# Kernel optimization log

Hardware: AMD Instinct MI355X
Metric: run time of the kernel (lower is better)

The kernel has to match this reference:

```python
import math
import jax, jax.numpy as jnp
import numpy as np

D, H, NB, L, K = 45, 256, 6, 2, 8          # features, hidden, maf blocks, made hidden layers, spline bins
M = 3 * K - 1                               # params per feature (tails='linear')
TAIL = -math.log(1e-6)                      # tail_bound = -log(alpha)
MIN_BW = MIN_BH = MIN_D = 1e-3


def _masks():
    # nflows MADE sequential degrees (random_mask=False)
    d_in = np.arange(1, D + 1)
    d_h = (np.arange(H) % (D - 1)) + 1
    m0 = (d_h[:, None] >= d_in[None, :]).astype(np.float32)   # [H, D]
    mh = (d_h[:, None] >= d_h[None, :]).astype(np.float32)    # [H, H]
    d_out = np.repeat(d_in, M)                                 # nflows tile(): each degree repeated M times
    mf = (d_out[:, None] > d_h[None, :]).astype(np.float32)   # [D*M, H], strict for output layer
    return jnp.asarray(m0), jnp.asarray(mh), jnp.asarray(mf)


def _rq_spline(x, params):
    # x: [B, D]; params: [B, D, M]. unconstrained_rational_quadratic_spline, tails='linear'.
    uw = params[..., :K] / math.sqrt(H)        # nflows divides by sqrt(hidden_features)
    uh = params[..., K:2 * K] / math.sqrt(H)
    const = math.log(math.exp(1.0 - MIN_D) - 1.0)
    ud = jnp.pad(params[..., 2 * K:], ((0, 0), (0, 0), (1, 1)), constant_values=const)  # [B,D,K+1]
    inside = (x >= -TAIL) & (x <= TAIL)
    xc = jnp.clip(x, -TAIL, TAIL)

    def bin_edges(u, mn):
        p = jax.nn.softmax(u, -1)
        p = mn + (1.0 - mn * K) * p
        c = jnp.pad(jnp.cumsum(p, -1), ((0, 0), (0, 0), (1, 0)))
        c = 2.0 * TAIL * c - TAIL
        c = c.at[..., 0].set(-TAIL).at[..., -1].set(TAIL)
        return c, c[..., 1:] - c[..., :-1]

    cw, w = bin_edges(uw, MIN_BW)              # cumwidths [B,D,K+1], widths [B,D,K]
    ch, h = bin_edges(uh, MIN_BH)
    d = MIN_D + jax.nn.softplus(ud)            # derivatives [B,D,K+1]

    idx = jnp.clip(jnp.sum((xc[..., None] >= cw), -1) - 1, 0, K - 1)[..., None]
    g = lambda a: jnp.take_along_axis(a, idx, -1)[..., 0]
    icw, ibw, ich, ih = g(cw[..., :-1]), g(w), g(ch[..., :-1]), g(h)
    idelta = g(h / w)
    id0, id1 = g(d[..., :-1]), g(d[..., 1:])

    th = (xc - icw) / ibw
    th1 = th * (1.0 - th)
    den = idelta + (id0 + id1 - 2.0 * idelta) * th1
    y = ich + ih * (idelta * th * th + id0 * th1) / den
    lad = jnp.log(idelta * idelta * (id1 * th * th + 2.0 * idelta * th1 + id0 * (1.0 - th) ** 2)) - 2.0 * jnp.log(den)
    return jnp.where(inside, y, x), jnp.where(inside, lad, 0.0)


def setup_inputs() -> dict:
    key = jax.random.key(0)
    ks = jax.random.split(key, 10)
    B, s = 32768, 0.02
    return {
        "x": jax.random.normal(ks[0], (B, D), jnp.float32),
        "cond": jax.random.normal(ks[1], (B, 1), jnp.float32),
        "W0": jax.random.normal(ks[2], (NB, H, D), jnp.float32) * s,
        "b0": jax.random.normal(ks[3], (NB, H), jnp.float32) * s,
        "Wc": jax.random.normal(ks[4], (NB, H, 1), jnp.float32) * s,
        "bc": jax.random.normal(ks[5], (NB, H), jnp.float32) * s,
        "Wh": jax.random.normal(ks[6], (NB, L, H, H), jnp.float32) * s,
        "bh": jax.random.normal(ks[7], (NB, L, H), jnp.float32) * s,
        "Wf": jax.random.normal(ks[8], (NB, D * M, H), jnp.float32) * s,
        "bf": jax.random.normal(ks[9], (NB, D * M), jnp.float32) * s,
    }


def reference(x, cond, W0, b0, Wc, bc, Wh, bh, Wf, bf):
    m0, mh, mf = _masks()
    z = x
    ld = jnp.zeros(x.shape[0], x.dtype)
    for b in range(NB):  # CompositeTransform of NB MAF blocks
        hid = z @ (W0[b] * m0).T + b0[b] + cond @ Wc[b].T + bc[b]
        for l in range(L):  # MaskedFeedforwardBlock: linear -> ReLU (dropout=0, no BN)
            hid = jax.nn.relu(hid @ (Wh[b, l] * mh).T + bh[b, l])
        params = (hid @ (Wf[b] * mf).T + bf[b]).reshape(z.shape[0], D, M)
        z, lad = _rq_spline(z, params)
        ld = ld + lad.sum(-1)
    log_z = 0.5 * D * math.log(2.0 * math.pi)
    return -0.5 * jnp.sum(z * z, axis=1) - log_z + ld
```

## Files before the change

kernel.cpp:

```cpp
#include <hip/hip_runtime.h>


typedef __bf16 bf16;
typedef __bf16 bf16x8 __attribute__((ext_vector_type(8)));
typedef float  f32x16 __attribute__((ext_vector_type(16)));

#define TAILF  13.815510557964274f
#define LOGZ   41.352233994210265f

#define WS_W0M   0
#define WS_WHM   196608
#define WS_WFM   1769472
#define WS_BEFF  5210112
#define WS_BFP   5216256
#define WS_WCC   5243136
#define WS_BHP   5249280
#define WS_NEED  5261568

#define N_W0  (6*256*64)
#define N_WH  (6*2*256*256)
#define N_WF  (6*5*224*256)
#define N_PREP (N_W0 + N_WH + N_WF)

__device__ __forceinline__ int s_deg(int s) {
    return (s < 216) ? (s / 6) : (36 + (s - 216) / 5);
}
__device__ __forceinline__ int s_orig(int s) {
    int d, rk;
    if (s < 216) { d = s / 6; rk = s - d * 6; }
    else { int u = s - 216; d = 36 + u / 5; rk = u - (u / 5) * 5; }
    return d + 44 * rk;
}

__global__ void prep_all(const float* __restrict__ W0, const float* __restrict__ b0,
                         const float* __restrict__ Wc, const float* __restrict__ bc,
                         const float* __restrict__ Wh, const float* __restrict__ Wf,
                         const float* __restrict__ bfv, const float* __restrict__ bh,
                         bf16* __restrict__ W0m, bf16* __restrict__ Whm,
                         bf16* __restrict__ Wfm,
                         float* __restrict__ beff, float* __restrict__ bfp,
                         float* __restrict__ Wcc, float* __restrict__ bhp)
{
    int idx = blockIdx.x * 256 + threadIdx.x;
    if (idx < N_W0) {
        int j = idx & 7, lane = (idx >> 3) & 63, chunk = idx >> 9;
        int kt = chunk & 3, cg = (chunk >> 2) & 7, b = chunk >> 5;
        int col = cg * 32 + (lane & 31);
        int k   = kt * 16 + (lane >> 5) * 8 + j;
        int o   = s_orig(col);
        float v = 0.f;
        if (k < 45 && s_deg(col) >= k)
            v = W0[(b * 256 + o) * 45 + k];
        W0m[idx] = (bf16)v;
        if (k == 0) {
            beff[b * 256 + col] = b0[b * 256 + o] + bc[b * 256 + o];
            Wcc[b * 256 + col]  = Wc[b * 256 + o];
        }
    } else if (idx < N_W0 + N_WH) {
        int id = idx - N_W0;
        int j = id & 7, lane = (id >> 3) & 63, chunk = id >> 9;
        int kt = chunk & 15, cg = (chunk >> 4) & 7, bl = chunk >> 7;
        int col = cg * 32 + (lane & 31);
        int k   = kt * 16 + (lane >> 5) * 8 + j;
        int oc  = s_orig(col), ok = s_orig(k);
        float v = (s_deg(col) >= s_deg(k)) ? Wh[bl * 65536 + oc * 256 + ok] : 0.f;
        Whm[id] = (bf16)v;
        if (k == 0)
            bhp[bl * 256 + col] = bh[bl * 256 + oc];
    } else if (idx < N_PREP) {
        int id = idx - (N_W0 + N_WH);
        int j = id & 7, lane = (id >> 3) & 63, chunk = id >> 9;
        int kt = chunk & 15, t2 = chunk >> 4;
        int cg = t2 % 7, bg = t2 / 7;
        int b  = bg / 5, g = bg - 5 * b;
        int col = cg * 32 + (lane & 31);
        int k   = kt * 16 + (lane >> 5) * 8 + j;
        int ok  = s_orig(k);
        int f   = 9 * g + col / 23;
        int m   = col - (col / 23) * 23;
        bool valid = (col < 207);
        float v = 0.f;
        if (valid && (f > s_deg(k)))
            v = Wf[(b * 1035 + f * 23 + m) * 256 + ok];
        Wfm[id] = (bf16)v;
        if (k == 0)
            bfp[bg * 224 + col] = valid ? bfv[b * 1035 + f * 23 + m] : 0.f;
    }
}

#define SO_ZF    0
#define SO_ZB    11776
#define SO_HIDA  18944
#define SO_PBUF  52736
#define SO_COND  80528
#define SO_LD    80784
#define SMEM_BYTES 81040

#define PBF 1544

__constant__ unsigned char HID_KT[8]    = {4,8,8,12,12,12,16,16};
__constant__ unsigned char OUT_KT[5][7] = {
    { 4, 4, 4, 4, 4, 4, 4},
    { 4, 8, 8, 8, 8, 8, 8},
    { 8, 8,12,12,12,12,12},
    {12,12,12,12,16,16,16},
    {16,16,16,16,16,16,16}};

template<int MODE>
__device__ __forceinline__ void epi32(const f32x16& acc, int cg, int hf,
    const float* __restrict__ bias, const float* __restrict__ wcol,
    const float* condl, bf16* dst, int l31, int kh8)
{
    const int col = cg * 32 + l31;
    if (MODE == 2 && col >= 207) return;
    const float bv = bias[col];
    const int rb = (kh8 >> 1) + hf * 32;
    if (MODE == 2) {
        const int fl = col / 23, m = col - fl * 23;
        bf16* dp = dst + fl * PBF + m;
        #pragma unroll
        for (int r = 0; r < 16; ++r) {
            int row = (r & 3) + 8 * (r >> 2) + rb;
            dp[row * 24] = (bf16)(acc[r] + bv);
        }
    } else {
        const float wcv = (MODE == 0) ? wcol[col] : 0.f;
        #pragma unroll
        for (int r = 0; r < 16; ++r) {
            int row = (r & 3) + 8 * (r >> 2) + rb;
            float v = acc[r] + bv;
            if (MODE == 0) v += condl[row] * wcv;
            if (MODE == 1) v = fmaxf(v, 0.f);
            dst[row * 264 + col] = (bf16)v;
        }
    }
}

template<int KTFULL, int MODE>
__device__ __forceinline__ void gemm64(
    const bf16* Asrc, const int lda,
    const bf16* __restrict__ Wp,
    const float* __restrict__ bias, const float* __restrict__ wcol,
    const float* condl, bf16* dst,
    int cg, int kt, int halfmask,
    int lane, bool preEpiSync)
{
    const int l31 = lane & 31;
    const int kh8 = (lane >> 5) * 8;
    const bf16* Bp  = Wp + (size_t)cg * (KTFULL * 512) + lane * 8;
    const bf16* Alo = Asrc + l31 * lda + kh8;
    const bf16* Ahi = Alo + 32 * lda;

    f32x16 acc0 = {}, acc1 = {};
    bf16x8 pA0, pA1, pA2, pA3, pB0, pB1, pB2, pB3;

#define LB(c)  (*reinterpret_cast<const bf16x8*>(Bp + (c) * 512))
#define LAL(c) (*reinterpret_cast<const bf16x8*>(Alo + (c) * 16))
#define LAH(c) (*reinterpret_cast<const bf16x8*>(Ahi + (c) * 16))
#define CHUNK(breg, c) { \
    bf16x8 a0_ = LAL(c), a1_ = LAH(c); \
    acc0 = __builtin_amdgcn_mfma_f32_32x32x16_bf16(a0_, breg, acc0, 0, 0, 0); \
    acc1 = __builtin_amdgcn_mfma_f32_32x32x16_bf16(a1_, breg, acc1, 0, 0, 0); }
#define LOADQ(r0, r1, r2, r3, q) { \
    r0 = LB((q)*4 + 0); r1 = LB((q)*4 + 1); \
    r2 = LB((q)*4 + 2); r3 = LB((q)*4 + 3); }
#define COMPQ(r0, r1, r2, r3, q) { \
    CHUNK(r0, (q)*4 + 0) CHUNK(r1, (q)*4 + 1) \
    CHUNK(r2, (q)*4 + 2) CHUNK(r3, (q)*4 + 3) }

    const int nq = __builtin_amdgcn_readfirstlane(kt >> 2);
    switch (nq) {
    case 1:
        LOADQ(pA0,pA1,pA2,pA3, 0);
        COMPQ(pA0,pA1,pA2,pA3, 0);
        break;
    case 2:
        LOADQ(pA0,pA1,pA2,pA3, 0); LOADQ(pB0,pB1,pB2,pB3, 1);
        COMPQ(pA0,pA1,pA2,pA3, 0); COMPQ(pB0,pB1,pB2,pB3, 1);
        break;
    case 3:
        LOADQ(pA0,pA1,pA2,pA3, 0); LOADQ(pB0,pB1,pB2,pB3, 1);
        COMPQ(pA0,pA1,pA2,pA3, 0); LOADQ(pA0,pA1,pA2,pA3, 2);
        COMPQ(pB0,pB1,pB2,pB3, 1); COMPQ(pA0,pA1,pA2,pA3, 2);
        break;
    default:
        LOADQ(pA0,pA1,pA2,pA3, 0); LOADQ(pB0,pB1,pB2,pB3, 1);
        COMPQ(pA0,pA1,pA2,pA3, 0); LOADQ(pA0,pA1,pA2,pA3, 2);
        COMPQ(pB0,pB1,pB2,pB3, 1); LOADQ(pB0,pB1,pB2,pB3, 3);
        COMPQ(pA0,pA1,pA2,pA3, 2); COMPQ(pB0,pB1,pB2,pB3, 3);
        break;
    }
#undef LB
#undef LAL
#undef LAH
#undef CHUNK
#undef LOADQ
#undef COMPQ

    if (preEpiSync) __syncthreads();

    if (halfmask & 1) epi32<MODE>(acc0, cg, 0, bias, wcol, condl, dst, l31, kh8);
    if (halfmask & 2) epi32<MODE>(acc1, cg, 1, bias, wcol, condl, dst, l31, kh8);
    __syncthreads();
}

__device__ __forceinline__ void do_spline9(int fb, float* zf, bf16* zb,
                                           const bf16* pbuf, int t, float& lad_acc)
{
    #pragma unroll 1
    for (int task = t; task < 576; task += 512) {
        int fl = task >> 6, r = task & 63;
        const bf16* pp = pbuf + fl * PBF + r * 24;
        bf16x8 q0 = *reinterpret_cast<const bf16x8*>(pp);
        bf16x8 q1 = *reinterpret_cast<const bf16x8*>(pp + 8);
        bf16x8 q2 = *reinterpret_cast<const bf16x8*>(pp + 16);
        float P[23];
        #pragma unroll
        for (int m = 0; m < 8; ++m) P[m]      = (float)q0[m];
        #pragma unroll
        for (int m = 0; m < 8; ++m) P[8 + m]  = (float)q1[m];
        #pragma unroll
        for (int m = 0; m < 7; ++m) P[16 + m] = (float)q2[m];

        float xin = zf[r * 46 + fb + fl];
        float xc  = fminf(fmaxf(xin, -TAILF), TAILF);
        bool inside = (xin >= -TAILF) && (xin <= TAILF);

        float mw = P[0];
        #pragma unroll
        for (int i = 1; i < 8; ++i) mw = fmaxf(mw, P[i]);
        float ew[8], sw = 0.f;
        #pragma unroll
        for (int i = 0; i < 8; ++i) { ew[i] = __expf((P[i] - mw) * 0.0625f); sw += ew[i]; }
        float rws = 0.992f / sw;
        float cw[9]; cw[0] = -TAILF;
        #pragma unroll
        for (int i = 0; i < 8; ++i)
            cw[i + 1] = cw[i] + 2.f * TAILF * (1e-3f + ew[i] * rws);
        cw[8] = TAILF;
        float wb[8];
        #pragma unroll
        for (int i = 0; i < 8; ++i) wb[i] = cw[i + 1] - cw[i];

        float mh = P[8];
        #pragma unroll
        for (int i = 1; i < 8; ++i) mh = fmaxf(mh, P[8 + i]);
        float eh[8], sh = 0.f;
        #pragma unroll
        for (int i = 0; i < 8; ++i) { eh[i] = __expf((P[8 + i] - mh) * 0.0625f); sh += eh[i]; }
        float rhs = 0.992f / sh;
        float ch[9]; ch[0] = -TAILF;
        #pragma unroll
        for (int i = 0; i < 8; ++i)
            ch[i + 1] = ch[i] + 2.f * TAILF * (1e-3f + eh[i] * rhs);
        ch[8] = TAILF;
        float hb[8];
        #pragma unroll
        for (int i = 0; i < 8; ++i) hb[i] = ch[i + 1] - ch[i];

        float dd[9];
        dd[0] = 1.0f; dd[8] = 1.0f;
        #pragma unroll
        for (int i = 1; i < 8; ++i)
            dd[i] = 1e-3f + __logf(1.f + __expf(P[15 + i]));

        float icw = cw[0], ich = ch[0], ibw = wb[0], ibh = hb[0];
        float id0 = dd[0], id1 = dd[1];
        #pragma unroll
        for (int i = 1; i < 8; ++i) {
            bool ge = xc >= cw[i];
            icw = ge ? cw[i] : icw;  ich = ge ? ch[i] : ich;
            ibw = ge ? wb[i] : ibw;  ibh = ge ? hb[i] : ibh;
            id0 = ge ? dd[i] : id0;  id1 = ge ? dd[i + 1] : id1;
        }

        float th  = (xc - icw) / ibw;
        float th1 = th * (1.f - th);
        float dl  = ibh / ibw;
        float den = dl + (id0 + id1 - 2.f * dl) * th1;
        float yy  = ich + ibh * (dl * th * th + id0 * th1) / den;
        float num = dl * dl * (id1 * th * th + 2.f * dl * th1
                               + id0 * (1.f - th) * (1.f - th));
        float lad = __logf(num) - 2.f * __logf(den);

        if (inside) {
            zf[r * 46 + fb + fl] = yy;
            zb[r * 56 + fb + fl] = (bf16)yy;
        }
        lad_acc += inside ? lad : 0.f;
    }
}

__global__ __launch_bounds__(512, 4) void maf_main(
    const float* __restrict__ x, const float* __restrict__ cond,
    const bf16* __restrict__ W0m, const bf16* __restrict__ Whm,
    const bf16* __restrict__ Wfm,
    const float* __restrict__ beff, const float* __restrict__ bfp,
    const float* __restrict__ Wcc, const float* __restrict__ bhp,
    float* __restrict__ out, int B)
{
    extern __shared__ char smem[];
    float* zf    = (float*)(smem + SO_ZF);
    bf16*  zb    = (bf16*)(smem + SO_ZB);
    bf16*  hidA  = (bf16*)(smem + SO_HIDA);
    bf16*  pbuf  = (bf16*)(smem + SO_PBUF);
    float* condl = (float*)(smem + SO_COND);
    float* ldl   = (float*)(smem + SO_LD);

    const int t    = threadIdx.x;
    const int r0   = blockIdx.x * 64;
    const int w    = t >> 6;
    const int lane = t & 63;
    const int wu   = __builtin_amdgcn_readfirstlane(w);

    for (int i = t; i < 64 * 11; i += 512) {
        int r = i / 11, c = i - (i / 11) * 11;
        zb[r * 56 + 45 + c] = (bf16)0.f;
    }
    for (int i = t; i < 64 * 45; i += 512) {
        int r = i / 45, f = i - (i / 45) * 45;
        float v = (r0 + r < B) ? x[(size_t)(r0 + r) * 45 + f] : 0.f;
        zf[r * 46 + f] = v;
        zb[r * 56 + f] = (bf16)v;
    }
    if (t < 64) {
        condl[t] = (r0 + t < B) ? cond[r0 + t] : 0.f;
        ldl[t]   = 0.f;
    }
    __syncthreads();

    float lad_acc = 0.f;

    const int hidKt = HID_KT[wu];
    const int ocg   = (wu <= 5) ? wu : 6;
    const int ohm   = (wu <= 5) ? 3 : ((wu == 6) ? 1 : 2);

    #pragma unroll 1
    for (int b = 0; b < 6; ++b) {
        gemm64<4, 0>(zb, 56, W0m + b * 16384,
                     beff + b * 256, Wcc + b * 256, condl,
                     hidA, wu, 4, 3, lane, false);
        #pragma unroll 1
        for (int l = 0; l < 2; ++l)
            gemm64<16, 1>(hidA, 264, Whm + (b * 2 + l) * 65536,
                          bhp + (b * 2 + l) * 256, nullptr, condl,
                          hidA, wu, hidKt, 3, lane, true);
        #pragma unroll 1
        for (int g = 0; g < 5; ++g) {
            gemm64<16, 2>(hidA, 264, Wfm + (size_t)(b * 5 + g) * 57344,
                          bfp + (b * 5 + g) * 224, nullptr, condl,
                          pbuf, ocg, OUT_KT[g][ocg], ohm, lane, false);
            do_spline9(g * 9, zf, zb, pbuf, t, lad_acc);
            __syncthreads();
        }
    }

    atomicAdd(&ldl[t & 63], lad_acc);
    __syncthreads();

    if (t < 64 && r0 + t < B) {
        float s = 0.f;
        #pragma unroll
        for (int f = 0; f < 45; ++f) { float v = zf[t * 46 + f]; s += v * v; }
        out[r0 + t] = -0.5f * s - LOGZ + ldl[t];
    }
}

extern "C" void kernel_launch(void* const* d_in, const int* in_sizes, int n_in,
                              void* d_out, int out_size, void* d_ws, size_t ws_size,
                              hipStream_t stream)
{
    const float* x    = (const float*)d_in[0];
    const float* cond = (const float*)d_in[1];
    const float* W0   = (const float*)d_in[2];
    const float* b0   = (const float*)d_in[3];
    const float* Wc   = (const float*)d_in[4];
    const float* bc   = (const float*)d_in[5];
    const float* Wh   = (const float*)d_in[6];
    const float* bh   = (const float*)d_in[7];
    const float* Wf   = (const float*)d_in[8];
    const float* bfv  = (const float*)d_in[9];
    float* out = (float*)d_out;

    const int B = in_sizes[0] / 45;
    if (ws_size < (size_t)WS_NEED) return;

    char* ws = (char*)d_ws;
    bf16*  W0m  = (bf16*)(ws + WS_W0M);
    bf16*  Whm  = (bf16*)(ws + WS_WHM);
    bf16*  Wfm  = (bf16*)(ws + WS_WFM);
    float* beff = (float*)(ws + WS_BEFF);
    float* bfp  = (float*)(ws + WS_BFP);
    float* Wcc  = (float*)(ws + WS_WCC);
    float* bhp  = (float*)(ws + WS_BHP);

    prep_all<<<(N_PREP + 255) / 256, 256, 0, stream>>>(
        W0, b0, Wc, bc, Wh, Wf, bfv, bh, W0m, Whm, Wfm, beff, bfp, Wcc, bhp);

    (void)hipFuncSetAttribute((const void*)maf_main,
                              hipFuncAttributeMaxDynamicSharedMemorySize,
                              SMEM_BYTES);

    const int nwg = (B + 63) / 64;
    maf_main<<<nwg, 512, SMEM_BYTES, stream>>>(
        x, cond, W0m, Whm, Wfm, beff, bfp, Wcc, bhp, out, B);
}
```

Baseline: 325.6 us.

## Overlap spline with next output GEMM and use pair-granular K trimming

Restructures the per-block schedule so the weight loads for output group g are issued before the spline for group g-1 runs. The spline work then hides global load latency, and the separate barrier after each spline is removed by using the GEMM's pre-epilogue sync. K-trimming moves from 4-chunk to 2-chunk granularity through new per-wave pair-count tables, which skips more of the masked zero work. The software-pipelined loop uses fewer registers but a runtime loop instead of fully unrolled cases, which may cost some scheduling quality.

```diff
diff --git a/kernel.cpp b/kernel.cpp
--- a/kernel.cpp
+++ b/kernel.cpp
@@ -98,13 +98,17 @@
 
 #define PBF 1544
 
-__constant__ unsigned char HID_KT[8]    = {4,8,8,12,12,12,16,16};
-__constant__ unsigned char OUT_KT[5][7] = {
-    { 4, 4, 4, 4, 4, 4, 4},
-    { 4, 8, 8, 8, 8, 8, 8},
-    { 8, 8,12,12,12,12,12},
-    {12,12,12,12,16,16,16},
-    {16,16,16,16,16,16,16}};
+__constant__ unsigned char IN_NP[8]     = {1,1,1,1,1,1,2,2};
+__constant__ unsigned char HID_NP[8]    = {2,3,3,5,6,6,8,8};
+__constant__ unsigned char OUT_NP[5][7] = {
+    {1,1,1,1,2,2,2},
+    {2,3,3,3,3,4,4},
+    {4,4,5,5,5,5,5},
+    {6,6,6,6,7,7,7},
+    {7,8,8,8,8,8,8}};
+
+__device__ __forceinline__ void do_spline9(int fb, float* zf, bf16* zb,
+                                           const bf16* pbuf, int t, float& lad_acc);
 
 template<int MODE>
 __device__ __forceinline__ void epi32(const f32x16& acc, int cg, int hf,
@@ -136,14 +140,15 @@
     }
 }
 
-template<int KTFULL, int MODE>
+template<int KTFULL, int MODE, bool SPLINE>
 __device__ __forceinline__ void gemm64(
     const bf16* Asrc, const int lda,
     const bf16* __restrict__ Wp,
     const float* __restrict__ bias, const float* __restrict__ wcol,
     const float* condl, bf16* dst,
-    int cg, int kt, int halfmask,
-    int lane, bool preEpiSync)
+    int cg, int np, int halfmask,
+    int lane, bool preEpiSync,
+    int fb, float* zf, bf16* zb, const bf16* pbuf, int t, float* lad_acc)
 {
     const int l31 = lane & 31;
     const int kh8 = (lane >> 5) * 8;
@@ -152,50 +157,42 @@
     const bf16* Ahi = Alo + 32 * lda;
 
     f32x16 acc0 = {}, acc1 = {};
-    bf16x8 pA0, pA1, pA2, pA3, pB0, pB1, pB2, pB3;
-
-#define LB(c)  (*reinterpret_cast<const bf16x8*>(Bp + (c) * 512))
+    bf16x8 rA0, rA1, rB0, rB1;
+
+#define LB(c)  (*reinterpret_cast<const bf16x8*>(Bp + (size_t)(c) * 512))
 #define LAL(c) (*reinterpret_cast<const bf16x8*>(Alo + (c) * 16))
 #define LAH(c) (*reinterpret_cast<const bf16x8*>(Ahi + (c) * 16))
 #define CHUNK(breg, c) { \
     bf16x8 a0_ = LAL(c), a1_ = LAH(c); \
     acc0 = __builtin_amdgcn_mfma_f32_32x32x16_bf16(a0_, breg, acc0, 0, 0, 0); \
     acc1 = __builtin_amdgcn_mfma_f32_32x32x16_bf16(a1_, breg, acc1, 0, 0, 0); }
-#define LOADQ(r0, r1, r2, r3, q) { \
-    r0 = LB((q)*4 + 0); r1 = LB((q)*4 + 1); \
-    r2 = LB((q)*4 + 2); r3 = LB((q)*4 + 3); }
-#define COMPQ(r0, r1, r2, r3, q) { \
-    CHUNK(r0, (q)*4 + 0) CHUNK(r1, (q)*4 + 1) \
-    CHUNK(r2, (q)*4 + 2) CHUNK(r3, (q)*4 + 3) }
-
-    const int nq = __builtin_amdgcn_readfirstlane(kt >> 2);
-    switch (nq) {
-    case 1:
-        LOADQ(pA0,pA1,pA2,pA3, 0);
-        COMPQ(pA0,pA1,pA2,pA3, 0);
-        break;
-    case 2:
-        LOADQ(pA0,pA1,pA2,pA3, 0); LOADQ(pB0,pB1,pB2,pB3, 1);
-        COMPQ(pA0,pA1,pA2,pA3, 0); COMPQ(pB0,pB1,pB2,pB3, 1);
-        break;
-    case 3:
-        LOADQ(pA0,pA1,pA2,pA3, 0); LOADQ(pB0,pB1,pB2,pB3, 1);
-        COMPQ(pA0,pA1,pA2,pA3, 0); LOADQ(pA0,pA1,pA2,pA3, 2);
-        COMPQ(pB0,pB1,pB2,pB3, 1); COMPQ(pA0,pA1,pA2,pA3, 2);
-        break;
-    default:
-        LOADQ(pA0,pA1,pA2,pA3, 0); LOADQ(pB0,pB1,pB2,pB3, 1);
-        COMPQ(pA0,pA1,pA2,pA3, 0); LOADQ(pA0,pA1,pA2,pA3, 2);
-        COMPQ(pB0,pB1,pB2,pB3, 1); LOADQ(pB0,pB1,pB2,pB3, 3);
-        COMPQ(pA0,pA1,pA2,pA3, 2); COMPQ(pB0,pB1,pB2,pB3, 3);
-        break;
-    }
+#define LP(r0, r1, p) { r0 = LB(2*(p)); r1 = LB(2*(p)+1); }
+#define CP(r0, r1, p) { CHUNK(r0, 2*(p)) CHUNK(r1, 2*(p)+1) }
+
+    LP(rA0, rA1, 0);
+    if (np > 1) LP(rB0, rB1, 1);
+
+    if constexpr (SPLINE)
+        do_spline9(fb, zf, zb, pbuf, t, *lad_acc);
+
+    int p = 0;
+    #pragma unroll 1
+    while (p + 2 < np) {
+        CP(rA0, rA1, p);
+        LP(rA0, rA1, p + 2);
+        CP(rB0, rB1, p + 1);
+        if (p + 3 < np) LP(rB0, rB1, p + 3);
+        p += 2;
+    }
+    CP(rA0, rA1, p);
+    if (np - p > 1) CP(rB0, rB1, p + 1);
+
 #undef LB
 #undef LAL
 #undef LAH
 #undef CHUNK
-#undef LOADQ
-#undef COMPQ
+#undef LP
+#undef CP
 
     if (preEpiSync) __syncthreads();
 
@@ -317,6 +314,7 @@
         int r = i / 11, c = i - (i / 11) * 11;
         zb[r * 56 + 45 + c] = (bf16)0.f;
     }
+    if (t < 8) hidA[t] = (bf16)0.f;
     for (int i = t; i < 64 * 45; i += 512) {
         int r = i / 45, f = i - (i / 45) * 45;
         float v = (r0 + r < B) ? x[(size_t)(r0 + r) * 45 + f] : 0.f;
@@ -331,28 +329,36 @@
 
     float lad_acc = 0.f;
 
-    const int hidKt = HID_KT[wu];
+    const int inNp  = IN_NP[wu];
+    const int hidNp = HID_NP[wu];
     const int ocg   = (wu <= 5) ? wu : 6;
     const int ohm   = (wu <= 5) ? 3 : ((wu == 6) ? 1 : 2);
 
     #pragma unroll 1
     for (int b = 0; b < 6; ++b) {
-        gemm64<4, 0>(zb, 56, W0m + b * 16384,
-                     beff + b * 256, Wcc + b * 256, condl,
-                     hidA, wu, 4, 3, lane, false);
+        gemm64<4, 0, false>(zb, 56, W0m + b * 16384,
+                            beff + b * 256, Wcc + b * 256, condl,
+                            hidA, wu, inNp, 3, lane, false,
+                            0, nullptr, nullptr, nullptr, 0, nullptr);
         #pragma unroll 1
         for (int l = 0; l < 2; ++l)
-            gemm64<16, 1>(hidA, 264, Whm + (b * 2 + l) * 65536,
-                          bhp + (b * 2 + l) * 256, nullptr, condl,
-                          hidA, wu, hidKt, 3, lane, true);
+            gemm64<16, 1, false>(hidA, 264, Whm + (b * 2 + l) * 65536,
+                                 bhp + (b * 2 + l) * 256, nullptr, condl,
+                                 hidA, wu, hidNp, 3, lane, true,
+                                 0, nullptr, nullptr, nullptr, 0, nullptr);
+        gemm64<16, 2, false>(hidA, 264, Wfm + (size_t)(b * 5) * 57344,
+                             bfp + (b * 5) * 224, nullptr, condl,
+                             pbuf, ocg, OUT_NP[0][ocg], ohm, lane, false,
+                             0, nullptr, nullptr, nullptr, 0, nullptr);
         #pragma unroll 1
-        for (int g = 0; g < 5; ++g) {
-            gemm64<16, 2>(hidA, 264, Wfm + (size_t)(b * 5 + g) * 57344,
-                          bfp + (b * 5 + g) * 224, nullptr, condl,
-                          pbuf, ocg, OUT_KT[g][ocg], ohm, lane, false);
-            do_spline9(g * 9, zf, zb, pbuf, t, lad_acc);
-            __syncthreads();
-        }
+        for (int g = 1; g < 5; ++g) {
+            gemm64<16, 2, true>(hidA, 264, Wfm + (size_t)(b * 5 + g) * 57344,
+                                bfp + (b * 5 + g) * 224, nullptr, condl,
+                                pbuf, ocg, OUT_NP[g][ocg], ohm, lane, true,
+                                (g - 1) * 9, zf, zb, pbuf, t, &lad_acc);
+        }
+        do_spline9(36, zf, zb, pbuf, t, lad_acc);
+        __syncthreads();
     }
 
     atomicAdd(&ldl[t & 63], lad_acc);
```

After: 320.8 us. No clear change (-1.5%).
